# Performance work log

Hardware: AMD Instinct MI355X
Metric: run time of the kernel (lower is better)

## Reference

```python
import jax, jax.numpy as jnp
import numpy as np
from jax import lax

KERNEL_SIZE = 2
DILATION = 1


def setup_inputs() -> dict:
    key = jax.random.key(0)
    k1, k2, k3, k4, k5 = jax.random.split(key, 5)
    bsz, h_size, seq_len = 8, 1024, 1024
    z1ss = jax.random.normal(k1, (bsz, 2 * h_size, seq_len), dtype=jnp.float32)
    uss = jax.random.normal(k2, (bsz, 4 * h_size, seq_len), dtype=jnp.float32)
    z0 = jax.random.normal(k3, (bsz, 2 * h_size, 1), dtype=jnp.float32)
    # conv params initialized ~ N(0, 0.01) as in init_weights
    weight = 0.01 * jax.random.normal(k4, (4 * h_size, h_size, KERNEL_SIZE), dtype=jnp.float32)
    bias = 0.01 * jax.random.normal(k5, (4 * h_size,), dtype=jnp.float32)
    return {"z1ss": z1ss, "uss": uss, "z0": z0, "weight": weight, "bias": bias}


def reference(z1ss, uss, z0, weight, bias):
    h_size = z1ss.shape[1] // 2
    z1h, z1c = z1ss[:, :h_size], z1ss[:, h_size:]          # (B, H, T) each
    z0h, z0c0 = z0[:, :h_size], z0[:, h_size:]             # (B, H, 1)
    # previous cell state: [z0c, z1c[..., :-1]]
    z0c = jnp.concatenate([z0c0, z1c], axis=2)[:, :, :-1]  # (B, H, T)
    # causal pad, injecting hid into the padded region
    pad = (KERNEL_SIZE - 1) * DILATION
    b = z1h.shape[0]
    hid = jnp.broadcast_to(z0h, (b, h_size, pad))
    xp = jnp.concatenate([hid, z1h], axis=2)               # (B, H, T+pad)
    conv = lax.conv_general_dilated(
        xp, weight, window_strides=(1,), padding='VALID',
        rhs_dilation=(DILATION,), dimension_numbers=('NCH', 'OIH', 'NCH'))
    out = uss + conv + bias[None, :, None]                 # (B, 4H, T)
    it, ot, gt, ft = jnp.split(out, 4, axis=1)
    it, ot, gt, ft = jax.nn.sigmoid(it), jax.nn.sigmoid(ot), jnp.tanh(gt), jax.nn.sigmoid(ft)
    ct = ft * z0c + it * gt
    ht = ot * jnp.tanh(ct)
    return jnp.concatenate([ht, ct], axis=1)               # (B, 2H, T)
```

## Files before the change

kernel.cpp:

```cpp
#include <hip/hip_runtime.h>
#include <hip/hip_bf16.h>
#include <cstdint>

#define HSZ   1024
#define SEQ   1024
#define NTOT  8192
#define K2    2048

typedef __attribute__((ext_vector_type(8))) short bf16x8;
typedef __attribute__((ext_vector_type(4))) float f32x4;

__device__ __forceinline__ unsigned f2bf(float x) {
  unsigned u = __builtin_bit_cast(unsigned, x);
  return (u + 0x7fffu + ((u >> 16) & 1u)) >> 16;
}
__device__ __forceinline__ float fsig(float x)  { return 1.f / (1.f + __expf(-x)); }
__device__ __forceinline__ float ftanh(float x) { return 1.f - 2.f / (__expf(2.f * x) + 1.f); }

__device__ __forceinline__ void gload_lds16(const void* g, void* l) {
  __builtin_amdgcn_global_load_lds(
      (const __attribute__((address_space(1))) unsigned*)g,
      (__attribute__((address_space(3))) unsigned*)l, 16, 0, 0);
}

__global__ void conv_weight_kernel(const float* __restrict__ w, unsigned* __restrict__ wb) {
  int idx = (blockIdx.x * 256 + threadIdx.x) * 4;
  f32x4 v = *(const f32x4*)(w + idx);
  uint2 o;
  o.x = f2bf(v.x) | (f2bf(v.y) << 16);
  o.y = f2bf(v.z) | (f2bf(v.w) << 16);
  *(uint2*)(wb + (idx >> 1)) = o;
}

__global__ void build_bdup_kernel(const float* __restrict__ z1ss, const float* __restrict__ z0,
                                  unsigned* __restrict__ bd) {
  __shared__ float tile[32 * 34];
  const int tid = threadIdx.x;
  const int n0 = blockIdx.x * 32;
  const int i0 = blockIdx.y * 32;
  const int b  = n0 >> 10;
  const int t0 = n0 & 1023;
  const int ii = tid >> 3, js = tid & 7;
  const float* zrow = z1ss + (b * 2048 + i0 + ii) * 1024;
  const float z0v = z0[b * 2048 + i0 + ii];
#pragma unroll
  for (int p = 0; p < 5; ++p) {
    int j = js + p * 8;
    if (j < 33) {
      int gt = t0 - 1 + j;
      tile[ii * 34 + j] = (gt < 0) ? z0v : zrow[gt];
    }
  }
  __syncthreads();
  const int i2 = tid & 31, ts = tid >> 5;
#pragma unroll
  for (int p = 0; p < 4; ++p) {
    int tt = ts + p * 8;
    float prev = tile[i2 * 34 + tt];
    float cur  = tile[i2 * 34 + tt + 1];
    bd[(n0 + tt) * 1024 + i0 + i2] = f2bf(prev) | (f2bf(cur) << 16);
  }
}

__launch_bounds__(256, 3)
__global__ void lstm_gemm_kernel(const unsigned short* __restrict__ Wb,
                                 const unsigned short* __restrict__ Bd,
                                 const float* __restrict__ uss,
                                 const float* __restrict__ z1ss,
                                 const float* __restrict__ z0,
                                 const float* __restrict__ bias,
                                 float* __restrict__ out) {
  __shared__ unsigned short Asm_[128 * 32];
  __shared__ unsigned short Bsm_[128 * 32];
  const int tid  = threadIdx.x;
  const int wave = tid >> 6, lane = tid & 63;
  const int l15  = lane & 15, quad = lane >> 4;
  const int c0 = blockIdx.y * 32;
  const int n0 = blockIdx.x * 128;

  const unsigned short* agp[2];
  const unsigned short* bgp[2];
#pragma unroll
  for (int j = 0; j < 2; ++j) {
    const int idx = (wave * 2 + j) * 64 + lane;
    const int row = idx >> 2;
    const int chunk = (idx & 3) ^ ((row >> 1) & 3);
    const int wrow = ((row >> 5) << 10) + c0 + (row & 31);
    agp[j] = Wb + (size_t)wrow * K2 + chunk * 8;
    bgp[j] = Bd + (size_t)(n0 + row) * K2 + chunk * 8;
  }
  unsigned short* ldsA[2] = { Asm_ + (wave * 2 + 0) * 512, Asm_ + (wave * 2 + 1) * 512 };
  unsigned short* ldsB[2] = { Bsm_ + (wave * 2 + 0) * 512, Bsm_ + (wave * 2 + 1) * 512 };

  const int swz  = (l15 >> 1) & 3;
  const int lofs = l15 * 32 + ((quad ^ swz) << 3);

  f32x4 acc[4][2][2];
#pragma unroll
  for (int g = 0; g < 4; ++g)
#pragma unroll
    for (int h = 0; h < 2; ++h)
#pragma unroll
      for (int nt = 0; nt < 2; ++nt)
        acc[g][h][nt] = (f32x4){0.f, 0.f, 0.f, 0.f};

  for (int k0 = 0; k0 < K2; k0 += 32) {
#pragma unroll
    for (int j = 0; j < 2; ++j) gload_lds16(agp[j] + k0, ldsA[j]);
#pragma unroll
    for (int j = 0; j < 2; ++j) gload_lds16(bgp[j] + k0, ldsB[j]);
    __syncthreads();

    bf16x8 bf[2];
#pragma unroll
    for (int nt = 0; nt < 2; ++nt)
      bf[nt] = *(const bf16x8*)(Bsm_ + wave * 1024 + nt * 512 + lofs);
#pragma unroll
    for (int g = 0; g < 4; ++g)
#pragma unroll
      for (int h = 0; h < 2; ++h) {
        const int mt = g * 2 + h;
        bf16x8 af = *(const bf16x8*)(Asm_ + mt * 512 + lofs);
#pragma unroll
        for (int nt = 0; nt < 2; ++nt)
          acc[g][h][nt] = __builtin_amdgcn_mfma_f32_16x16x32_bf16(af, bf[nt], acc[g][h][nt], 0, 0, 0);
      }
    __syncthreads();
  }

#pragma unroll
  for (int h = 0; h < 2; ++h) {
#pragma unroll
    for (int r = 0; r < 4; ++r) {
      const int c = c0 + h * 16 + quad * 4 + r;
      const float bv0 = bias[c], bv1 = bias[1024 + c], bv2 = bias[2048 + c], bv3 = bias[3072 + c];
#pragma unroll
      for (int nt = 0; nt < 2; ++nt) {
        const int n = n0 + wave * 32 + nt * 16 + l15;
        const int b = n >> 10, t = n & 1023;
        const int ub = b * 4194304 + c * 1024 + t;
        float p0 = acc[0][h][nt][r] + uss[ub]           + bv0;
        float p1 = acc[1][h][nt][r] + uss[ub + 1048576] + bv1;
        float p2 = acc[2][h][nt][r] + uss[ub + 2097152] + bv2;
        float p3 = acc[3][h][nt][r] + uss[ub + 3145728] + bv3;
        float it = fsig(p0), ot = fsig(p1), g_ = ftanh(p2), ft = fsig(p3);
        float zc = t ? z1ss[(b * 2048 + 1024 + c) * 1024 + t - 1]
                     : z0[b * 2048 + 1024 + c];
        float ct = ft * zc + it * g_;
        float ht = ot * ftanh(ct);
        const int ob = (b * 2048 + c) * 1024 + t;
        out[ob] = ht;
        out[ob + 1048576] = ct;
      }
    }
  }
}

__global__ void naive_kernel(const float* __restrict__ z1ss, const float* __restrict__ uss,
                             const float* __restrict__ z0, const float* __restrict__ w,
                             const float* __restrict__ bias, float* __restrict__ out) {
  int idx = blockIdx.x * 256 + threadIdx.x;
  int b = idx >> 20, c = (idx >> 10) & 1023, t = idx & 1023;
  float s0 = 0.f, s1 = 0.f, s2 = 0.f, s3 = 0.f;
  const float* xb = z1ss + b * 2097152;
  for (int i = 0; i < 1024; ++i) {
    float cur  = xb[i * 1024 + t];
    float prev = t ? xb[i * 1024 + t - 1] : z0[b * 2048 + i];
    const float* wr = w + c * 2048 + i * 2;
    s0 += wr[0]       * prev + wr[1]       * cur;
    s1 += wr[2097152] * prev + wr[2097153] * cur;
    s2 += wr[4194304] * prev + wr[4194305] * cur;
    s3 += wr[6291456] * prev + wr[6291457] * cur;
  }
  int ub = b * 4194304 + c * 1024 + t;
  float p0 = s0 + uss[ub]           + bias[c];
  float p1 = s1 + uss[ub + 1048576] + bias[1024 + c];
  float p2 = s2 + uss[ub + 2097152] + bias[2048 + c];
  float p3 = s3 + uss[ub + 3145728] + bias[3072 + c];
  float it = fsig(p0), ot = fsig(p1), g_ = ftanh(p2), ft = fsig(p3);
  float zc = t ? z1ss[(b * 2048 + 1024 + c) * 1024 + t - 1] : z0[b * 2048 + 1024 + c];
  float ct = ft * zc + it * g_;
  float ht = ot * ftanh(ct);
  int ob = (b * 2048 + c) * 1024 + t;
  out[ob] = ht;
  out[ob + 1048576] = ct;
}

extern "C" void kernel_launch(void* const* d_in, const int* in_sizes, int n_in,
                              void* d_out, int out_size, void* d_ws, size_t ws_size,
                              hipStream_t stream) {
  const float* z1ss = (const float*)d_in[0];
  const float* uss  = (const float*)d_in[1];
  const float* z0   = (const float*)d_in[2];
  const float* w    = (const float*)d_in[3];
  const float* bias = (const float*)d_in[4];
  float* out = (float*)d_out;

  const size_t needWb = (size_t)4096 * 2048 * 2;
  const size_t needBd = (size_t)NTOT * K2 * 2;
  if (ws_size >= needWb + needBd) {
    unsigned short* Wb = (unsigned short*)d_ws;
    unsigned short* Bd = Wb + (size_t)4096 * 2048;
    conv_weight_kernel<<<8192, 256, 0, stream>>>(w, (unsigned*)Wb);
    build_bdup_kernel<<<dim3(256, 32), 256, 0, stream>>>(z1ss, z0, (unsigned*)Bd);
    lstm_gemm_kernel<<<dim3(64, 32), 256, 0, stream>>>(Wb, Bd, uss, z1ss, z0, bias, out);
  } else {
    naive_kernel<<<32768, 256, 0, stream>>>(z1ss, uss, z0, w, bias, out);
  }
}
```

Baseline: 453.1 us.

## Rewrite LSTM GEMM with 256x256 tiles and a 4-stage LDS pipeline

```diff
diff --git a/kernel.cpp b/kernel.cpp
--- a/kernel.cpp
+++ b/kernel.cpp
@@ -9,6 +9,9 @@
 
 typedef __attribute__((ext_vector_type(8))) short bf16x8;
 typedef __attribute__((ext_vector_type(4))) float f32x4;
+
+#define WAITVM(N) asm volatile("s_waitcnt vmcnt(" #N ")" ::: "memory")
+#define LGKM0     asm volatile("s_waitcnt lgkmcnt(0)" ::: "memory")
 
 __device__ __forceinline__ unsigned f2bf(float x) {
   unsigned u = __builtin_bit_cast(unsigned, x);
@@ -62,7 +65,63 @@
   }
 }
 
-__launch_bounds__(256, 3)
+template<int BUF, int VMN, bool STG>
+__device__ __forceinline__ void tile_step(
+    unsigned short* __restrict__ ldsA, unsigned short* __restrict__ ldsB,
+    const unsigned short*& aG0, const unsigned short*& aG1,
+    const unsigned short*& bG0, const unsigned short*& bG1,
+    const int sA0, const int sA1, const int aread, const int bread,
+    f32x4 (&acc)[8][4])
+{
+  constexpr int SB = (BUF + 3) & 3;
+  const unsigned short* Ab = ldsA + BUF * 8192 + aread;
+  const unsigned short* Bb = ldsB + BUF * 8192 + bread;
+  bf16x8 afr[4], bfr[4];
+
+  if constexpr (STG) {
+    gload_lds16(aG0, ldsA + SB * 8192 + sA0);
+    gload_lds16(bG0, ldsB + SB * 8192 + sA0);
+  }
+#pragma unroll
+  for (int nt = 0; nt < 4; ++nt) bfr[nt] = *(const bf16x8*)(Bb + nt * 512);
+#pragma unroll
+  for (int m = 0; m < 4; ++m)    afr[m]  = *(const bf16x8*)(Ab + m * 512);
+  __builtin_amdgcn_s_barrier();
+  LGKM0;
+  __builtin_amdgcn_sched_barrier(0);
+  __builtin_amdgcn_s_setprio(1);
+#pragma unroll
+  for (int m = 0; m < 4; ++m)
+#pragma unroll
+    for (int nt = 0; nt < 4; ++nt)
+      acc[m][nt] = __builtin_amdgcn_mfma_f32_16x16x32_bf16(afr[m], bfr[nt], acc[m][nt], 0, 0, 0);
+  __builtin_amdgcn_s_setprio(0);
+  __builtin_amdgcn_s_barrier();
+
+  if constexpr (STG) {
+    gload_lds16(aG1, ldsA + SB * 8192 + sA1);
+    gload_lds16(bG1, ldsB + SB * 8192 + sA1);
+    aG0 += 32; aG1 += 32; bG0 += 32; bG1 += 32;
+  }
+#pragma unroll
+  for (int m = 0; m < 4; ++m) afr[m] = *(const bf16x8*)(Ab + (m + 4) * 512);
+  if constexpr (VMN == 8)      WAITVM(8);
+  else if constexpr (VMN == 4) WAITVM(4);
+  else if constexpr (VMN == 0) WAITVM(0);
+  __builtin_amdgcn_s_barrier();
+  LGKM0;
+  __builtin_amdgcn_sched_barrier(0);
+  __builtin_amdgcn_s_setprio(1);
+#pragma unroll
+  for (int m = 0; m < 4; ++m)
+#pragma unroll
+    for (int nt = 0; nt < 4; ++nt)
+      acc[m + 4][nt] = __builtin_amdgcn_mfma_f32_16x16x32_bf16(afr[m], bfr[nt], acc[m + 4][nt], 0, 0, 0);
+  __builtin_amdgcn_s_setprio(0);
+  __builtin_amdgcn_s_barrier();
+}
+
+__launch_bounds__(512, 2)
 __global__ void lstm_gemm_kernel(const unsigned short* __restrict__ Wb,
                                  const unsigned short* __restrict__ Bd,
                                  const float* __restrict__ uss,
@@ -70,87 +129,94 @@
                                  const float* __restrict__ z0,
                                  const float* __restrict__ bias,
                                  float* __restrict__ out) {
-  __shared__ unsigned short Asm_[128 * 32];
-  __shared__ unsigned short Bsm_[128 * 32];
+  __shared__ unsigned short ldsA[4 * 8192];
+  __shared__ unsigned short ldsB[4 * 8192];
   const int tid  = threadIdx.x;
-  const int wave = tid >> 6, lane = tid & 63;
+  const int w    = tid >> 6, lane = tid & 63;
   const int l15  = lane & 15, quad = lane >> 4;
-  const int c0 = blockIdx.y * 32;
-  const int n0 = blockIdx.x * 128;
-
-  const unsigned short* agp[2];
-  const unsigned short* bgp[2];
-#pragma unroll
-  for (int j = 0; j < 2; ++j) {
-    const int idx = (wave * 2 + j) * 64 + lane;
-    const int row = idx >> 2;
-    const int chunk = (idx & 3) ^ ((row >> 1) & 3);
-    const int wrow = ((row >> 5) << 10) + c0 + (row & 31);
-    agp[j] = Wb + (size_t)wrow * K2 + chunk * 8;
-    bgp[j] = Bd + (size_t)(n0 + row) * K2 + chunk * 8;
-  }
-  unsigned short* ldsA[2] = { Asm_ + (wave * 2 + 0) * 512, Asm_ + (wave * 2 + 1) * 512 };
-  unsigned short* ldsB[2] = { Bsm_ + (wave * 2 + 0) * 512, Bsm_ + (wave * 2 + 1) * 512 };
-
-  const int swz  = (l15 >> 1) & 3;
-  const int lofs = l15 * 32 + ((quad ^ swz) << 3);
-
-  f32x4 acc[4][2][2];
-#pragma unroll
-  for (int g = 0; g < 4; ++g)
-#pragma unroll
-    for (int h = 0; h < 2; ++h)
-#pragma unroll
-      for (int nt = 0; nt < 2; ++nt)
-        acc[g][h][nt] = (f32x4){0.f, 0.f, 0.f, 0.f};
-
-  for (int k0 = 0; k0 < K2; k0 += 32) {
-#pragma unroll
-    for (int j = 0; j < 2; ++j) gload_lds16(agp[j] + k0, ldsA[j]);
-#pragma unroll
-    for (int j = 0; j < 2; ++j) gload_lds16(bgp[j] + k0, ldsB[j]);
-    __syncthreads();
-
-    bf16x8 bf[2];
-#pragma unroll
-    for (int nt = 0; nt < 2; ++nt)
-      bf[nt] = *(const bf16x8*)(Bsm_ + wave * 1024 + nt * 512 + lofs);
-#pragma unroll
-    for (int g = 0; g < 4; ++g)
-#pragma unroll
-      for (int h = 0; h < 2; ++h) {
-        const int mt = g * 2 + h;
-        bf16x8 af = *(const bf16x8*)(Asm_ + mt * 512 + lofs);
-#pragma unroll
-        for (int nt = 0; nt < 2; ++nt)
-          acc[g][h][nt] = __builtin_amdgcn_mfma_f32_16x16x32_bf16(af, bf[nt], acc[g][h][nt], 0, 0, 0);
-      }
-    __syncthreads();
-  }
-
-#pragma unroll
-  for (int h = 0; h < 2; ++h) {
-#pragma unroll
-    for (int r = 0; r < 4; ++r) {
-      const int c = c0 + h * 16 + quad * 4 + r;
-      const float bv0 = bias[c], bv1 = bias[1024 + c], bv2 = bias[2048 + c], bv3 = bias[3072 + c];
-#pragma unroll
-      for (int nt = 0; nt < 2; ++nt) {
-        const int n = n0 + wave * 32 + nt * 16 + l15;
-        const int b = n >> 10, t = n & 1023;
-        const int ub = b * 4194304 + c * 1024 + t;
-        float p0 = acc[0][h][nt][r] + uss[ub]           + bv0;
-        float p1 = acc[1][h][nt][r] + uss[ub + 1048576] + bv1;
-        float p2 = acc[2][h][nt][r] + uss[ub + 2097152] + bv2;
-        float p3 = acc[3][h][nt][r] + uss[ub + 3145728] + bv3;
+  const int wm   = w >> 2, wn = w & 3;
+
+  const int bid = blockIdx.x;
+  const int wg  = (bid & 7) * 64 + (bid >> 3);
+  const int c0  = (wg & 15) * 64;
+  const int n0  = (wg >> 4) * 256;
+
+  const int sA0 = (w * 2 + 0) * 512;
+  const int sA1 = (w * 2 + 1) * 512;
+  const unsigned short *aG0, *aG1, *bG0, *bG1;
+  {
+    const int u0 = (w * 2 + 0) * 64 + lane;
+    const int r0 = u0 >> 2;
+    const int k0c = ((u0 & 3) ^ ((r0 >> 1) & 3)) * 8;
+    const int wr0 = ((r0 >> 5) & 3) * 1024 + c0 + (r0 >> 7) * 32 + (r0 & 31);
+    aG0 = Wb + (size_t)wr0 * K2 + k0c;
+    bG0 = Bd + (size_t)(n0 + r0) * K2 + k0c;
+    const int u1 = (w * 2 + 1) * 64 + lane;
+    const int r1 = u1 >> 2;
+    const int k1c = ((u1 & 3) ^ ((r1 >> 1) & 3)) * 8;
+    const int wr1 = ((r1 >> 5) & 3) * 1024 + c0 + (r1 >> 7) * 32 + (r1 & 31);
+    aG1 = Wb + (size_t)wr1 * K2 + k1c;
+    bG1 = Bd + (size_t)(n0 + r1) * K2 + k1c;
+  }
+
+  const int swz   = (l15 >> 1) & 3;
+  const int lofs  = l15 * 32 + ((quad ^ swz) << 3);
+  const int aread = wm * 4096 + lofs;
+  const int bread = wn * 2048 + lofs;
+
+  f32x4 acc[8][4];
+#pragma unroll
+  for (int m = 0; m < 8; ++m)
+#pragma unroll
+    for (int nt = 0; nt < 4; ++nt)
+      acc[m][nt] = (f32x4){0.f, 0.f, 0.f, 0.f};
+
+#pragma unroll
+  for (int t = 0; t < 3; ++t) {
+    gload_lds16(aG0 + t * 32, ldsA + t * 8192 + sA0);
+    gload_lds16(aG1 + t * 32, ldsA + t * 8192 + sA1);
+    gload_lds16(bG0 + t * 32, ldsB + t * 8192 + sA0);
+    gload_lds16(bG1 + t * 32, ldsB + t * 8192 + sA1);
+  }
+  aG0 += 96; aG1 += 96; bG0 += 96; bG1 += 96;
+  WAITVM(8);
+  __builtin_amdgcn_s_barrier();
+
+  for (int it = 0; it < 15; ++it) {
+    tile_step<0, 8, true>(ldsA, ldsB, aG0, aG1, bG0, bG1, sA0, sA1, aread, bread, acc);
+    tile_step<1, 8, true>(ldsA, ldsB, aG0, aG1, bG0, bG1, sA0, sA1, aread, bread, acc);
+    tile_step<2, 8, true>(ldsA, ldsB, aG0, aG1, bG0, bG1, sA0, sA1, aread, bread, acc);
+    tile_step<3, 8, true>(ldsA, ldsB, aG0, aG1, bG0, bG1, sA0, sA1, aread, bread, acc);
+  }
+  tile_step<0, 8, true >(ldsA, ldsB, aG0, aG1, bG0, bG1, sA0, sA1, aread, bread, acc);
+  tile_step<1, 4, false>(ldsA, ldsB, aG0, aG1, bG0, bG1, sA0, sA1, aread, bread, acc);
+  tile_step<2, 0, false>(ldsA, ldsB, aG0, aG1, bG0, bG1, sA0, sA1, aread, bread, acc);
+  tile_step<3, -1, false>(ldsA, ldsB, aG0, aG1, bG0, bG1, sA0, sA1, aread, bread, acc);
+
+  const int nbase = n0 + wn * 64 + l15;
+#pragma unroll
+  for (int nt = 0; nt < 4; ++nt) {
+    const int n = nbase + nt * 16;
+    const int b = n >> 10, t = n & 1023;
+    const float* ussb = uss + (size_t)b * 4194304 + t;
+    const int zoff = b * 2048 + 1024;
+#pragma unroll
+    for (int cp = 0; cp < 2; ++cp) {
+#pragma unroll
+      for (int r = 0; r < 4; ++r) {
+        const int ch = c0 + wm * 32 + cp * 16 + quad * 4 + r;
+        float p0 = acc[0 + cp][nt][r] + ussb[(size_t)ch * 1024]          + bias[ch];
+        float p1 = acc[2 + cp][nt][r] + ussb[(size_t)(1024 + ch) * 1024] + bias[1024 + ch];
+        float p2 = acc[4 + cp][nt][r] + ussb[(size_t)(2048 + ch) * 1024] + bias[2048 + ch];
+        float p3 = acc[6 + cp][nt][r] + ussb[(size_t)(3072 + ch) * 1024] + bias[3072 + ch];
         float it = fsig(p0), ot = fsig(p1), g_ = ftanh(p2), ft = fsig(p3);
-        float zc = t ? z1ss[(b * 2048 + 1024 + c) * 1024 + t - 1]
-                     : z0[b * 2048 + 1024 + c];
+        float zc = t ? z1ss[(size_t)(zoff + ch) * 1024 + t - 1]
+                     : z0[zoff + ch];
         float ct = ft * zc + it * g_;
         float ht = ot * ftanh(ct);
-        const int ob = (b * 2048 + c) * 1024 + t;
-        out[ob] = ht;
-        out[ob + 1048576] = ct;
+        float* ob = out + (size_t)(b * 2048 + ch) * 1024 + t;
+        ob[0] = ht;
+        ob[1048576] = ct;
       }
     }
   }
@@ -203,7 +269,7 @@
     unsigned short* Bd = Wb + (size_t)4096 * 2048;
     conv_weight_kernel<<<8192, 256, 0, stream>>>(w, (unsigned*)Wb);
     build_bdup_kernel<<<dim3(256, 32), 256, 0, stream>>>(z1ss, z0, (unsigned*)Bd);
-    lstm_gemm_kernel<<<dim3(64, 32), 256, 0, stream>>>(Wb, Bd, uss, z1ss, z0, bias, out);
+    lstm_gemm_kernel<<<dim3(512), dim3(512), 0, stream>>>(Wb, Bd, uss, z1ss, z0, bias, out);
   } else {
     naive_kernel<<<32768, 256, 0, stream>>>(z1ss, uss, z0, w, bias, out);
   }
```

Result: slower. 511.4 us (+12.9%).

## Triple-buffer LDS with async global-to-LDS prefetch two k-steps ahead

Applied to the files above, without the earlier changes.

```diff
diff --git a/kernel.cpp b/kernel.cpp
--- a/kernel.cpp
+++ b/kernel.cpp
@@ -9,6 +9,8 @@
 
 typedef __attribute__((ext_vector_type(8))) short bf16x8;
 typedef __attribute__((ext_vector_type(4))) float f32x4;
+
+#define WAITVM(N) asm volatile("s_waitcnt vmcnt(" #N ")" ::: "memory")
 
 __device__ __forceinline__ unsigned f2bf(float x) {
   unsigned u = __builtin_bit_cast(unsigned, x);
@@ -69,31 +71,82 @@
                                  const float* __restrict__ z1ss,
                                  const float* __restrict__ z0,
                                  const float* __restrict__ bias,
+                                 float* __restrict__ out);
+
+template<int BUF, int SB, int VMN>
+__device__ __forceinline__ void kstep(
+    unsigned short* __restrict__ Asm_, unsigned short* __restrict__ Bsm_,
+    const unsigned short* aG0, const unsigned short* aG1,
+    const unsigned short* bG0, const unsigned short* bG1,
+    int kofs, int wave, int l15, int slotOfs,
+    f32x4 (&acc)[4][2][2])
+{
+  if constexpr (SB >= 0) {
+    unsigned short* la0 = Asm_ + SB * 4096 + (wave * 2 + 0) * 512;
+    unsigned short* la1 = Asm_ + SB * 4096 + (wave * 2 + 1) * 512;
+    unsigned short* lb0 = Bsm_ + SB * 4096 + (wave * 2 + 0) * 512;
+    unsigned short* lb1 = Bsm_ + SB * 4096 + (wave * 2 + 1) * 512;
+    gload_lds16(aG0 + kofs, la0);
+    gload_lds16(aG1 + kofs, la1);
+    gload_lds16(bG0 + kofs, lb0);
+    gload_lds16(bG1 + kofs, lb1);
+  }
+  const unsigned short* At = Asm_ + BUF * 4096;
+  const unsigned short* Bt = Bsm_ + BUF * 4096;
+  bf16x8 bf[2];
+#pragma unroll
+  for (int nt = 0; nt < 2; ++nt)
+    bf[nt] = *(const bf16x8*)(Bt + (wave * 32 + nt * 16 + l15) * 32 + slotOfs);
+#pragma unroll
+  for (int g = 0; g < 4; ++g)
+#pragma unroll
+    for (int h = 0; h < 2; ++h) {
+      bf16x8 af = *(const bf16x8*)(At + ((g * 2 + h) * 16 + l15) * 32 + slotOfs);
+#pragma unroll
+      for (int nt = 0; nt < 2; ++nt)
+        acc[g][h][nt] = __builtin_amdgcn_mfma_f32_16x16x32_bf16(af, bf[nt], acc[g][h][nt], 0, 0, 0);
+    }
+  if constexpr (VMN == 4) WAITVM(4);
+  else if constexpr (VMN == 0) WAITVM(0);
+  if constexpr (VMN >= 0) {
+    __builtin_amdgcn_s_barrier();
+    __builtin_amdgcn_sched_barrier(0);
+  }
+}
+
+__launch_bounds__(256, 3)
+__global__ void lstm_gemm_kernel(const unsigned short* __restrict__ Wb,
+                                 const unsigned short* __restrict__ Bd,
+                                 const float* __restrict__ uss,
+                                 const float* __restrict__ z1ss,
+                                 const float* __restrict__ z0,
+                                 const float* __restrict__ bias,
                                  float* __restrict__ out) {
-  __shared__ unsigned short Asm_[128 * 32];
-  __shared__ unsigned short Bsm_[128 * 32];
+  __shared__ unsigned short Asm_[3 * 4096];
+  __shared__ unsigned short Bsm_[3 * 4096];
   const int tid  = threadIdx.x;
   const int wave = tid >> 6, lane = tid & 63;
   const int l15  = lane & 15, quad = lane >> 4;
   const int c0 = blockIdx.y * 32;
   const int n0 = blockIdx.x * 128;
 
-  const unsigned short* agp[2];
-  const unsigned short* bgp[2];
-#pragma unroll
-  for (int j = 0; j < 2; ++j) {
-    const int idx = (wave * 2 + j) * 64 + lane;
-    const int row = idx >> 2;
-    const int chunk = (idx & 3) ^ ((row >> 1) & 3);
-    const int wrow = ((row >> 5) << 10) + c0 + (row & 31);
-    agp[j] = Wb + (size_t)wrow * K2 + chunk * 8;
-    bgp[j] = Bd + (size_t)(n0 + row) * K2 + chunk * 8;
-  }
-  unsigned short* ldsA[2] = { Asm_ + (wave * 2 + 0) * 512, Asm_ + (wave * 2 + 1) * 512 };
-  unsigned short* ldsB[2] = { Bsm_ + (wave * 2 + 0) * 512, Bsm_ + (wave * 2 + 1) * 512 };
-
-  const int swz  = (l15 >> 1) & 3;
-  const int lofs = l15 * 32 + ((quad ^ swz) << 3);
+  const unsigned short *aG0, *aG1, *bG0, *bG1;
+  {
+    const int u0 = (wave * 2 + 0) * 64 + lane;
+    const int r0 = u0 >> 2;
+    const int c0k = ((u0 & 3) ^ ((r0 >> 1) & 3)) * 8;
+    const int wr0 = (r0 >> 5) * 1024 + c0 + (r0 & 31);
+    aG0 = Wb + (size_t)wr0 * K2 + c0k;
+    bG0 = Bd + (size_t)(n0 + r0) * K2 + c0k;
+    const int u1 = (wave * 2 + 1) * 64 + lane;
+    const int r1 = u1 >> 2;
+    const int c1k = ((u1 & 3) ^ ((r1 >> 1) & 3)) * 8;
+    const int wr1 = (r1 >> 5) * 1024 + c0 + (r1 & 31);
+    aG1 = Wb + (size_t)wr1 * K2 + c1k;
+    bG1 = Bd + (size_t)(n0 + r1) * K2 + c1k;
+  }
+
+  const int slotOfs = ((quad ^ ((l15 >> 1) & 3)) << 3);
 
   f32x4 acc[4][2][2];
 #pragma unroll
@@ -104,29 +157,29 @@
       for (int nt = 0; nt < 2; ++nt)
         acc[g][h][nt] = (f32x4){0.f, 0.f, 0.f, 0.f};
 
-  for (int k0 = 0; k0 < K2; k0 += 32) {
-#pragma unroll
-    for (int j = 0; j < 2; ++j) gload_lds16(agp[j] + k0, ldsA[j]);
-#pragma unroll
-    for (int j = 0; j < 2; ++j) gload_lds16(bgp[j] + k0, ldsB[j]);
-    __syncthreads();
-
-    bf16x8 bf[2];
-#pragma unroll
-    for (int nt = 0; nt < 2; ++nt)
-      bf[nt] = *(const bf16x8*)(Bsm_ + wave * 1024 + nt * 512 + lofs);
-#pragma unroll
-    for (int g = 0; g < 4; ++g)
-#pragma unroll
-      for (int h = 0; h < 2; ++h) {
-        const int mt = g * 2 + h;
-        bf16x8 af = *(const bf16x8*)(Asm_ + mt * 512 + lofs);
-#pragma unroll
-        for (int nt = 0; nt < 2; ++nt)
-          acc[g][h][nt] = __builtin_amdgcn_mfma_f32_16x16x32_bf16(af, bf[nt], acc[g][h][nt], 0, 0, 0);
-      }
-    __syncthreads();
-  }
+  gload_lds16(aG0,      Asm_ + 0 * 4096 + (wave * 2 + 0) * 512);
+  gload_lds16(aG1,      Asm_ + 0 * 4096 + (wave * 2 + 1) * 512);
+  gload_lds16(bG0,      Bsm_ + 0 * 4096 + (wave * 2 + 0) * 512);
+  gload_lds16(bG1,      Bsm_ + 0 * 4096 + (wave * 2 + 1) * 512);
+  gload_lds16(aG0 + 32, Asm_ + 1 * 4096 + (wave * 2 + 0) * 512);
+  gload_lds16(aG1 + 32, Asm_ + 1 * 4096 + (wave * 2 + 1) * 512);
+  gload_lds16(bG0 + 32, Bsm_ + 1 * 4096 + (wave * 2 + 0) * 512);
+  gload_lds16(bG1 + 32, Bsm_ + 1 * 4096 + (wave * 2 + 1) * 512);
+  WAITVM(4);
+  __builtin_amdgcn_s_barrier();
+  __builtin_amdgcn_sched_barrier(0);
+
+  int kofs = 2 * 32;
+  for (int it = 0; it < 20; ++it) {
+    kstep<0, 2, 4>(Asm_, Bsm_, aG0, aG1, bG0, bG1, kofs,      wave, l15, slotOfs, acc);
+    kstep<1, 0, 4>(Asm_, Bsm_, aG0, aG1, bG0, bG1, kofs + 32, wave, l15, slotOfs, acc);
+    kstep<2, 1, 4>(Asm_, Bsm_, aG0, aG1, bG0, bG1, kofs + 64, wave, l15, slotOfs, acc);
+    kofs += 96;
+  }
+  kstep<0, 2, 4>(Asm_, Bsm_, aG0, aG1, bG0, bG1, kofs,      wave, l15, slotOfs, acc);
+  kstep<1, 0, 4>(Asm_, Bsm_, aG0, aG1, bG0, bG1, kofs + 32, wave, l15, slotOfs, acc);
+  kstep<2, -1, 0>(Asm_, Bsm_, aG0, aG1, bG0, bG1, 0, wave, l15, slotOfs, acc);
+  kstep<0, -1, -1>(Asm_, Bsm_, aG0, aG1, bG0, bG1, 0, wave, l15, slotOfs, acc);
 
 #pragma unroll
   for (int h = 0; h < 2; ++h) {
```

Measured after the change: 454.0 us. Within noise of the previous version (+0.2%).
